# Optimization experiments

Hardware: AMD Instinct MI355X
Metric: run time of the kernel (lower is better)

The kernel has to match this reference:

```python
import jax, jax.numpy as jnp
import numpy as np

T, B, E, H = 1024, 2, 1024, 16
D = E // H  # head_dim = 64
R = 2 * T - 1  # relative position range


def setup_inputs() -> dict:
    key = jax.random.key(0)
    ks = jax.random.split(key, 8)
    std = (2.0 / (E + E)) ** 0.5  # matches nn.init.normal_ std in reset_parameters
    return {
        "x": jax.random.normal(ks[0], (T, B, E), jnp.float32),
        "pos": jax.random.normal(ks[1], (R, 1, E), jnp.float32),
        "in_proj_weight": jax.random.normal(ks[2], (3 * E, E), jnp.float32) * std,
        "in_proj_bias": jnp.zeros((3 * E,), jnp.float32),
        "pos_proj_weight": jax.random.normal(ks[3], (E, E), jnp.float32) * std,
        "pos_proj_bias": jnp.zeros((E,), jnp.float32),
        "out_proj_weight": jax.random.normal(ks[4], (E, E), jnp.float32) * std,
        "out_proj_bias": jnp.zeros((E,), jnp.float32),
        "r_w_bias": jax.random.normal(ks[5], (H, D), jnp.float32) * 0.02,
        "r_r_bias": jax.random.normal(ks[6], (H, D), jnp.float32) * 0.02,
    }


def _rel_shift(x):
    """Transformer-XL relative shift. x: [b, h, q, r] -> shifted [b, h, q, r]."""
    b, h, q, r = x.shape
    zp = jnp.zeros((b, h, q, 1), x.dtype)
    xp = jnp.concatenate([zp, x], axis=3)          # [b, h, q, r+1]
    xp = xp.reshape(b, h, r + 1, q)[:, :, 1:, :]   # drop first row
    return xp.reshape(b, h, q, r)


def reference(x, pos, in_proj_weight, in_proj_bias, pos_proj_weight,
              pos_proj_bias, out_proj_weight, out_proj_bias, r_w_bias, r_r_bias):
    t, b, e = x.shape
    h, d = r_w_bias.shape
    # fused QKV projection: [T, B, 3E]
    qkv = x @ in_proj_weight.T + in_proj_bias
    q, k, v = jnp.split(qkv, 3, axis=-1)
    q = q.reshape(t, b, h, d)
    k = k.reshape(t, b, h, d)
    v = v.reshape(t, b, h, d)
    # position projection: [R, 1, E] -> [R, h, d]
    p = (pos @ pos_proj_weight.T + pos_proj_bias).reshape(-1, h, d)
    scale = 1.0 / jnp.sqrt(jnp.asarray(d, x.dtype))
    # content score AC: (q + r_w_bias) @ k^T
    ac = jnp.einsum('tbhd,sbhd->bhts', q + r_w_bias, k)
    # position score BD: (q + r_r_bias) @ pos^T, then relative shift
    bd = jnp.einsum('tbhd,rhd->bhtr', q + r_r_bias, p)
    bd = _rel_shift(bd)[..., :t]                    # keep klen columns
    attn = jax.nn.softmax((ac + bd) * scale, axis=-1)  # [b, h, t, s]
    ctx = jnp.einsum('bhts,sbhd->tbhd', attn, v).reshape(t, b, e)
    return ctx @ out_proj_weight.T + out_proj_bias
```

## Files before the change

### kernel.cpp

```cpp
#include <hip/hip_runtime.h>
#include <hip/hip_bf16.h>

#define TT 1024
#define BB 2
#define EE 1024
#define HH 16
#define DD 64
#define RR 2047
#define TB (TT * BB)
#define E3 (3 * EE)

#define AS1 __attribute__((address_space(1)))
#define AS3 __attribute__((address_space(3)))

typedef __attribute__((ext_vector_type(4))) float f32x4;
typedef __attribute__((ext_vector_type(8))) short s16x8;

static __device__ __forceinline__ short f2bf(float x) {
  unsigned u = __builtin_bit_cast(unsigned, x);
  unsigned r = (u + 0x7FFFu + ((u >> 16) & 1u)) >> 16;
  return (short)r;
}
static __device__ __forceinline__ float bf2f(short x) {
  unsigned u = ((unsigned)(unsigned short)x) << 16;
  return __builtin_bit_cast(float, u);
}
static __device__ __forceinline__ float bperm(int idx, float v) {
  return __builtin_bit_cast(float,
      __builtin_amdgcn_ds_bpermute(idx, __builtin_bit_cast(int, v)));
}
static __device__ __forceinline__ float exp2g(float x) {
  return __builtin_amdgcn_exp2f(x);
}

__global__ __launch_bounds__(256) void cvt_all(
    const float* __restrict__ x, const float* __restrict__ in_w,
    const float* __restrict__ pos, const float* __restrict__ pos_w,
    const float* __restrict__ out_w,
    short* __restrict__ xb, short* __restrict__ inwb, short* __restrict__ posb,
    short* __restrict__ poswb, short* __restrict__ outwb) {
  const long M1 = 1 << 20;
  long off = (long)(blockIdx.x * 256 + threadIdx.x) * 8;
  const float* src; short* dst; long nsrc;
  if (off < 2 * M1)      { src = x;     dst = xb;    nsrc = 2 * M1; }
  else if (off < 5 * M1) { off -= 2 * M1; src = in_w;  dst = inwb;  nsrc = 3 * M1; }
  else if (off < 7 * M1) { off -= 5 * M1; src = pos;   dst = posb;  nsrc = (long)RR * EE; }
  else if (off < 8 * M1) { off -= 7 * M1; src = pos_w; dst = poswb; nsrc = M1; }
  else                   { off -= 8 * M1; src = out_w; dst = outwb; nsrc = M1; }
  s16x8 o;
  if (off + 8 <= nsrc) {
    f32x4 a = *(const f32x4*)&src[off];
    f32x4 c = *(const f32x4*)&src[off + 4];
    #pragma unroll
    for (int j = 0; j < 4; ++j) { o[j] = f2bf(a[j]); o[4 + j] = f2bf(c[j]); }
  } else {
    #pragma unroll
    for (int j = 0; j < 8; ++j) o[j] = 0;
  }
  *(s16x8*)&dst[off] = o;
}

#define GBK 64

template <int BM, int BN, int WR, int WC, int OUT_BF16>
__device__ __forceinline__ void gemm_body(
    const short* __restrict__ A, const short* __restrict__ W,
    const float* __restrict__ bias, void* __restrict__ Cout,
    int M, int N, int K, int m0, int n0,
    short* __restrict__ vtout, int vtflag) {
  __shared__ __align__(16) short lA[2][BM * GBK];
  __shared__ __align__(16) short lB[2][BN * GBK];
  constexpr int MT = BM / WR / 16;
  constexpr int NT = BN / WC / 16;

  const int tid = threadIdx.x;
  const int lane = tid & 63;
  const int wv = tid >> 6;
  const int g = lane >> 4, cc = lane & 15;
  const int wr = wv / WC, wc = wv % WC;

  f32x4 acc[MT][NT];
  #pragma unroll
  for (int i = 0; i < MT; ++i)
    #pragma unroll
    for (int j = 0; j < NT; ++j) acc[i][j] = (f32x4){0.f, 0.f, 0.f, 0.f};

  auto stage = [&](int kk, int buf) {
    #pragma unroll
    for (int s = 0; s < BM / 32; ++s) {
      int c = s * 256 + tid;
      int row = c >> 3, c8 = c & 7;
      int k8 = c8 ^ (row & 7);
      __builtin_amdgcn_global_load_lds(
          (const AS1 void*)(A + (size_t)(m0 + row) * K + kk + k8 * 8),
          (AS3 void*)&lA[buf][c * 8], 16, 0, 0);
    }
    #pragma unroll
    for (int s = 0; s < BN / 32; ++s) {
      int c = s * 256 + tid;
      int row = c >> 3, c8 = c & 7;
      int k8 = c8 ^ (row & 7);
      __builtin_amdgcn_global_load_lds(
          (const AS1 void*)(W + (size_t)(n0 + row) * K + kk + k8 * 8),
          (AS3 void*)&lB[buf][c * 8], 16, 0, 0);
    }
  };

  int cur = 0;
  const int nt = K / GBK;
  stage(0, 0);

  #pragma unroll 1
  for (int t = 0; t < nt; ++t) {
    __syncthreads();
    if (t + 1 < nt) stage((t + 1) * GBK, cur ^ 1);

    s16x8 af[MT][2], bf[NT][2];
    #pragma unroll
    for (int mt = 0; mt < MT; ++mt) {
      int row = (BM / WR) * wr + 16 * mt + cc;
      #pragma unroll
      for (int kh = 0; kh < 2; ++kh)
        af[mt][kh] = *(const s16x8*)&lA[cur][row * GBK + (((4 * kh + g) ^ (row & 7)) * 8)];
    }
    #pragma unroll
    for (int ntc = 0; ntc < NT; ++ntc) {
      int col = (BN / WC) * wc + 16 * ntc + cc;
      #pragma unroll
      for (int kh = 0; kh < 2; ++kh)
        bf[ntc][kh] = *(const s16x8*)&lB[cur][col * GBK + (((4 * kh + g) ^ (col & 7)) * 8)];
    }
    #pragma unroll
    for (int kh = 0; kh < 2; ++kh)
      #pragma unroll
      for (int mt = 0; mt < MT; ++mt)
        #pragma unroll
        for (int ntc = 0; ntc < NT; ++ntc)
          acc[mt][ntc] = __builtin_amdgcn_mfma_f32_16x16x32_bf16(
              af[mt][kh], bf[ntc][kh], acc[mt][ntc], 0, 0, 0);
    cur ^= 1;
  }

  #pragma unroll
  for (int ntc = 0; ntc < NT; ++ntc) {
    int col = n0 + (BN / WC) * wc + 16 * ntc + cc;
    float bv = bias[col];
    #pragma unroll
    for (int mt = 0; mt < MT; ++mt)
      #pragma unroll
      for (int r = 0; r < 4; ++r) {
        int rowg = m0 + (BM / WR) * wr + 16 * mt + 4 * g + r;
        float val = acc[mt][ntc][r] + bv;
        if (OUT_BF16) {
          if (vtflag) {
            const int cv = col - 2048;
            const int hh = cv >> 6, dd = cv & 63;
            vtout[((size_t)((rowg & 1) * 16 + hh) * 64 + dd) * TT + (rowg >> 1)] =
                f2bf(val);
          } else {
            ((short*)Cout)[(size_t)rowg * N + col] = f2bf(val);
          }
        } else {
          ((float*)Cout)[(size_t)rowg * N + col] = val;
        }
      }
  }
}

__global__ __launch_bounds__(256) void gemm_qkv_pos(
    const short* __restrict__ xb, const short* __restrict__ inwb,
    const float* __restrict__ in_b, short* __restrict__ qkvb,
    const short* __restrict__ posb, const short* __restrict__ poswb,
    const float* __restrict__ pos_b, short* __restrict__ pb,
    short* __restrict__ vTb) {
  const int bid = blockIdx.x;
  const short *A, *W; const float* bias; short* C; int N, m0, n0, vtf;
  if (bid < 384) {
    A = xb; W = inwb; bias = in_b; C = qkvb; N = E3;
    n0 = (bid % 24) * 128; m0 = (bid / 24) * 128;
    vtf = (n0 >= 2048) ? 1 : 0;
  } else {
    const int i = bid - 384;
    A = posb; W = poswb; bias = pos_b; C = pb; N = EE;
    n0 = (i % 8) * 128; m0 = (i / 8) * 128;
    vtf = 0;
  }
  gemm_body<128, 128, 2, 2, 1>(A, W, bias, C, TB, N, EE, m0, n0, vTb, vtf);
}

__global__ __launch_bounds__(256) void gemm_out(
    const short* __restrict__ ctxb, const short* __restrict__ outwb,
    const float* __restrict__ out_b, float* __restrict__ out) {
  gemm_body<128, 64, 4, 1, 0>(ctxb, outwb, out_b, out, TB, EE, EE,
                              blockIdx.y * 128, blockIdx.x * 64, nullptr, 0);
}

__global__ __launch_bounds__(512, 4) void rel_attn_mfma9(
    const short* __restrict__ qkvb,
    const short* __restrict__ pb,
    const short* __restrict__ vT,
    const float* __restrict__ rwb,
    const float* __restrict__ rrb,
    short* __restrict__ ctxb) {
  __shared__ __align__(16) char arena[68608];

  const int tid = threadIdx.x;
  const int wv = tid >> 6;
  const int qsub = wv & 3, ksub = wv >> 2;
  const int lane = tid & 63;
  const int g = lane >> 4, cc = lane & 15;

  const int bid = blockIdx.x;
  const int bh = (bid & 7) * 4 + (bid >> 7);
  const int qx = (bid >> 3) & 15;
  const int iq0 = qx * 64;
  const int b = bh >> 4, h = bh & 15;
  const int hoff = h * DD;
  const int n0p = 15 - qx;

  short* sPm = (short*)(arena + 57344 + wv * 1280);

  const float qscale = 0.125f * 1.44269504088896f;
  s16x8 qw[2], qr[2];
  #pragma unroll
  for (int kh = 0; kh < 2; ++kh) {
    const int d0 = 32 * kh + 8 * g;
    const short* qp = qkvb + (size_t)((iq0 + 16 * qsub + cc) * BB + b) * E3 + hoff + d0;
    const float* rw = rwb + hoff + d0;
    const float* rr = rrb + hoff + d0;
    s16x8 qv = *(const s16x8*)qp;
    #pragma unroll
    for (int j = 0; j < 8; ++j) {
      float q = bf2f(qv[j]);
      qw[kh][j] = f2bf((q + rw[j]) * qscale);
      qr[kh][j] = f2bf((q + rr[j]) * qscale);
    }
  }

  f32x4 O[4];
  #pragma unroll
  for (int dt = 0; dt < 4; ++dt) O[dt] = (f32x4){0.f, 0.f, 0.f, 0.f};
  float mrun[4], lpart[4];
  #pragma unroll
  for (int r = 0; r < 4; ++r) { mrun[r] = -1e30f; lpart[r] = 0.f; }

#define STAGE_KV(t_, buf_)                                                     \
  {                                                                            \
    const int j0s = (t_) * 64;                                                 \
    const int row = tid >> 3, c8 = tid & 7;                                    \
    const int swz = (c8 ^ (row & 7)) * 8;                                      \
    __builtin_amdgcn_global_load_lds(                                          \
        (const AS1 void*)(qkvb + (size_t)((j0s + row) * BB + b) * E3 + EE + hoff + swz), \
        (AS3 void*)(arena + (buf_) * 8192 + tid * 16), 16, 0, 0);              \
    __builtin_amdgcn_global_load_lds(                                          \
        (const AS1 void*)(vT + (size_t)(bh * DD + row) * TT + j0s + swz),      \
        (AS3 void*)(arena + 16384 + (buf_) * 8192 + tid * 16), 16, 0, 0);      \
  }
#define STAGE_P(p_)                                                            \
  {                                                                            \
    const int row = tid >> 3, c8 = tid & 7;                                    \
    const int swz = (c8 ^ (row & 7)) * 8;                                      \
    __builtin_amdgcn_global_load_lds(                                          \
        (const AS1 void*)(pb + (size_t)((p_) * 64 + row) * EE + hoff + swz),   \
        (AS3 void*)(arena + 32768 + ((p_) % 3) * 8192 + tid * 16), 16, 0, 0);  \
  }

  int cur = 0;
  int sl0 = n0p % 3, sl1 = (n0p + 1) % 3;
  STAGE_KV(0, 0);
  STAGE_P(n0p);
  STAGE_P(n0p + 1);

  #pragma unroll 1
  for (int t = 0; t < 16; ++t) {
    __syncthreads();
    if (t + 1 < 16) {
      STAGE_KV(t + 1, cur ^ 1);
      STAGE_P(n0p + t + 2);
    }

    short* ldsK = (short*)(arena + cur * 8192);
    short* ldsV = (short*)(arena + 16384 + cur * 8192);

    s16x8 kf[2][2];
    #pragma unroll
    for (int ct = 0; ct < 2; ++ct)
      #pragma unroll
      for (int kh = 0; kh < 2; ++kh) {
        const int row = 32 * ksub + 16 * ct + cc;
        kf[ct][kh] = *(const s16x8*)&ldsK[row * 64 + (((g + 4 * kh) ^ (row & 7)) * 8)];
      }

    f32x4 S[2];
    #pragma unroll
    for (int ct = 0; ct < 2; ++ct) {
      S[ct] = (f32x4){0.f, 0.f, 0.f, 0.f};
      #pragma unroll
      for (int kh = 0; kh < 2; ++kh)
        S[ct] = __builtin_amdgcn_mfma_f32_16x16x32_bf16(qw[kh], kf[ct][kh], S[ct], 0, 0, 0);
    }

    const int bbase = 32 * ksub - 16 * qsub + 48;
    f32x4 bt[3];
    #pragma unroll
    for (int ut = 0; ut < 3; ++ut) {
      const int rel = bbase + 16 * ut + cc;
      const int rr = rel & 63;
      const short* pp_ = (const short*)(arena + 32768 +
                                        ((rel >= 64) ? sl1 : sl0) * 8192);
      bt[ut] = (f32x4){0.f, 0.f, 0.f, 0.f};
      #pragma unroll
      for (int kh = 0; kh < 2; ++kh) {
        s16x8 pf = *(const s16x8*)&pp_[rr * 64 + (((g + 4 * kh) ^ (rr & 7)) * 8)];
        bt[ut] = __builtin_amdgcn_mfma_f32_16x16x32_bf16(qr[kh], pf, bt[ut], 0, 0, 0);
      }
    }
    #pragma unroll
    for (int r = 0; r < 4; ++r) {
      const int usub = cc + 15 - 4 * g - r;
      const int idx = ((lane & 48) | (usub & 15)) << 2;
      const float va = bperm(idx, bt[0][r]);
      const float vb = bperm(idx, bt[1][r]);
      const float vc = bperm(idx, bt[2][r]);
      const bool hi = usub >= 16;
      S[0][r] += hi ? vb : va;
      S[1][r] += hi ? vc : vb;
    }

    float mx[4];
    #pragma unroll
    for (int r = 0; r < 4; ++r) mx[r] = fmaxf(S[0][r], S[1][r]);
    const bool need = (mx[0] > mrun[0]) || (mx[1] > mrun[1]) ||
                      (mx[2] > mrun[2]) || (mx[3] > mrun[3]);
    if (__any(need)) {
      #pragma unroll
      for (int msk = 1; msk < 16; msk <<= 1)
        #pragma unroll
        for (int r = 0; r < 4; ++r) mx[r] = fmaxf(mx[r], __shfl_xor(mx[r], msk, 64));
      #pragma unroll
      for (int r = 0; r < 4; ++r) {
        const float mn = fmaxf(mrun[r], mx[r]);
        const float f = exp2g(mrun[r] - mn);
        mrun[r] = mn;
        lpart[r] *= f;
        #pragma unroll
        for (int dt = 0; dt < 4; ++dt) O[dt][r] *= f;
      }
    }
    #pragma unroll
    for (int r = 0; r < 4; ++r) {
      S[0][r] = exp2g(S[0][r] - mrun[r]);
      S[1][r] = exp2g(S[1][r] - mrun[r]);
      lpart[r] += S[0][r] + S[1][r];
    }

    #pragma unroll
    for (int ct = 0; ct < 2; ++ct)
      #pragma unroll
      for (int r = 0; r < 4; ++r)
        sPm[(4 * g + r) * 40 + 16 * ct + cc] = f2bf(S[ct][r]);

    s16x8 pa = *(const s16x8*)&sPm[cc * 40 + 8 * g];

    #pragma unroll
    for (int dt = 0; dt < 4; ++dt) {
      const int row = 16 * dt + cc;
      s16x8 vf = *(const s16x8*)&ldsV[row * 64 + (((4 * ksub + g) ^ (row & 7)) * 8)];
      O[dt] = __builtin_amdgcn_mfma_f32_16x16x32_bf16(pa, vf, O[dt], 0, 0, 0);
    }

    cur ^= 1;
    const int sln = (sl1 + 1) - (((sl1 + 1) >= 3) ? 3 : 0);
    sl0 = sl1;
    sl1 = sln;
  }
#undef STAGE_KV
#undef STAGE_P

  #pragma unroll
  for (int msk = 1; msk < 16; msk <<= 1)
    #pragma unroll
    for (int r = 0; r < 4; ++r) lpart[r] += __shfl_xor(lpart[r], msk, 64);

  __syncthreads();

  float* sOw = (float*)(arena + wv * 4352);
  #pragma unroll
  for (int dt = 0; dt < 4; ++dt)
    #pragma unroll
    for (int r = 0; r < 4; ++r)
      sOw[(4 * g + r) * 68 + 16 * dt + cc] = O[dt][r];
  float* sML = (float*)(arena + 67584);
  if (cc == 0) {
    #pragma unroll
    for (int r = 0; r < 4; ++r) {
      sML[wv * 32 + (4 * g + r)] = mrun[r];
      sML[wv * 32 + 16 + (4 * g + r)] = lpart[r];
    }
  }
  __syncthreads();

  const int ii = tid >> 3;
  const int ii_l = ii & 15;
  const int w0 = ii >> 4, w1 = w0 + 4;
  const int c0 = (tid & 7) * 8;
  const float m0 = sML[w0 * 32 + ii_l], l0 = sML[w0 * 32 + 16 + ii_l];
  const float m1 = sML[w1 * 32 + ii_l], l1 = sML[w1 * 32 + 16 + ii_l];
  const float M = fmaxf(m0, m1);
  const float f0 = exp2g(m0 - M), f1 = exp2g(m1 - M);
  const float rinv = 1.0f / (f0 * l0 + f1 * l1);
  const float* sO0 = (const float*)(arena + w0 * 4352);
  const float* sO1 = (const float*)(arena + w1 * 4352);
  s16x8 ov;
  #pragma unroll
  for (int jj = 0; jj < 8; ++jj) {
    const float val = (f0 * sO0[ii_l * 68 + c0 + jj] + f1 * sO1[ii_l * 68 + c0 + jj]) * rinv;
    ov[jj] = f2bf(val);
  }
  *(s16x8*)(ctxb + (size_t)((iq0 + ii) * BB + b) * EE + hoff + c0) = ov;
}

extern "C" void kernel_launch(void* const* d_in, const int* in_sizes, int n_in,
                              void* d_out, int out_size, void* d_ws, size_t ws_size,
                              hipStream_t stream) {
  const float* x      = (const float*)d_in[0];
  const float* pos    = (const float*)d_in[1];
  const float* in_w   = (const float*)d_in[2];
  const float* in_b   = (const float*)d_in[3];
  const float* pos_w  = (const float*)d_in[4];
  const float* pos_b  = (const float*)d_in[5];
  const float* out_w  = (const float*)d_in[6];
  const float* out_b  = (const float*)d_in[7];
  const float* r_w    = (const float*)d_in[8];
  const float* r_r    = (const float*)d_in[9];
  float* out = (float*)d_out;

  const size_t M1 = 1024 * 1024;
  short* xb    = (short*)d_ws;
  short* inwb  = xb    + 2 * M1;
  short* posb  = inwb  + 3 * M1;
  short* poswb = posb  + 2 * M1;
  short* outwb = poswb + 1 * M1;
  short* qkvb  = outwb + 1 * M1;
  short* pb    = qkvb  + 6 * M1;
  short* ctxb  = pb    + 2 * M1;
  short* vTb   = ctxb  + 2 * M1;

  cvt_all<<<dim3(4608), dim3(256), 0, stream>>>(
      x, in_w, pos, pos_w, out_w, xb, inwb, posb, poswb, outwb);

  gemm_qkv_pos<<<dim3(512), dim3(256), 0, stream>>>(
      xb, inwb, in_b, qkvb, posb, poswb, pos_b, pb, vTb);

  rel_attn_mfma9<<<dim3(512), dim3(512), 0, stream>>>(
      qkvb, pb, vTb, r_w, r_r, ctxb);

  gemm_out<<<dim3(EE / 64, TB / 128), dim3(256), 0, stream>>>(
      ctxb, outwb, out_b, out);
}
```

Measured before the change: 102.6 us.

## Give each attention wave two query tiles with 256-thread blocks

The relative attention kernel drops from 8 waves to 4 per block. Each wave now handles 32 query rows as two 16-row tiles instead of one, so K, V and position fragments read from LDS are reused across both tiles, and the position fragments are shared between overlapping BD tiles (4 loads instead of 6). Staging loops are doubled so fewer threads cover the same tiles. The cost is higher register pressure and fewer waves per block to hide latency.

```diff
diff --git a/kernel.cpp b/kernel.cpp
--- a/kernel.cpp
+++ b/kernel.cpp
@@ -195,7 +195,7 @@
                               blockIdx.y * 128, blockIdx.x * 64, nullptr, 0);
 }
 
-__global__ __launch_bounds__(512, 4) void rel_attn_mfma9(
+__global__ __launch_bounds__(256) void rel_attn_mfma10(
     const short* __restrict__ qkvb,
     const short* __restrict__ pb,
     const short* __restrict__ vT,
@@ -206,7 +206,7 @@
 
   const int tid = threadIdx.x;
   const int wv = tid >> 6;
-  const int qsub = wv & 3, ksub = wv >> 2;
+  const int qsub = wv >> 1, ksub = wv & 1;
   const int lane = tid & 63;
   const int g = lane >> 4, cc = lane & 15;
 
@@ -218,51 +218,65 @@
   const int hoff = h * DD;
   const int n0p = 15 - qx;
 
-  short* sPm = (short*)(arena + 57344 + wv * 1280);
+  short* sPm = (short*)(arena + 57344 + wv * 2560);
 
   const float qscale = 0.125f * 1.44269504088896f;
-  s16x8 qw[2], qr[2];
-  #pragma unroll
-  for (int kh = 0; kh < 2; ++kh) {
-    const int d0 = 32 * kh + 8 * g;
-    const short* qp = qkvb + (size_t)((iq0 + 16 * qsub + cc) * BB + b) * E3 + hoff + d0;
-    const float* rw = rwb + hoff + d0;
-    const float* rr = rrb + hoff + d0;
-    s16x8 qv = *(const s16x8*)qp;
-    #pragma unroll
-    for (int j = 0; j < 8; ++j) {
-      float q = bf2f(qv[j]);
-      qw[kh][j] = f2bf((q + rw[j]) * qscale);
-      qr[kh][j] = f2bf((q + rr[j]) * qscale);
-    }
-  }
-
-  f32x4 O[4];
-  #pragma unroll
-  for (int dt = 0; dt < 4; ++dt) O[dt] = (f32x4){0.f, 0.f, 0.f, 0.f};
-  float mrun[4], lpart[4];
-  #pragma unroll
-  for (int r = 0; r < 4; ++r) { mrun[r] = -1e30f; lpart[r] = 0.f; }
+  s16x8 qw[2][2], qr[2][2];
+  #pragma unroll
+  for (int qt = 0; qt < 2; ++qt)
+    #pragma unroll
+    for (int kh = 0; kh < 2; ++kh) {
+      const int d0 = 32 * kh + 8 * g;
+      const short* qp = qkvb + (size_t)((iq0 + 32 * qsub + 16 * qt + cc) * BB + b) * E3 + hoff + d0;
+      const float* rw = rwb + hoff + d0;
+      const float* rr = rrb + hoff + d0;
+      s16x8 qv = *(const s16x8*)qp;
+      #pragma unroll
+      for (int j = 0; j < 8; ++j) {
+        float q = bf2f(qv[j]);
+        qw[qt][kh][j] = f2bf((q + rw[j]) * qscale);
+        qr[qt][kh][j] = f2bf((q + rr[j]) * qscale);
+      }
+    }
+
+  f32x4 O[2][4];
+  #pragma unroll
+  for (int qt = 0; qt < 2; ++qt)
+    #pragma unroll
+    for (int dt = 0; dt < 4; ++dt) O[qt][dt] = (f32x4){0.f, 0.f, 0.f, 0.f};
+  float mrun[2][4], lpart[2][4];
+  #pragma unroll
+  for (int qt = 0; qt < 2; ++qt)
+    #pragma unroll
+    for (int r = 0; r < 4; ++r) { mrun[qt][r] = -1e30f; lpart[qt][r] = 0.f; }
 
 #define STAGE_KV(t_, buf_)                                                     \
   {                                                                            \
     const int j0s = (t_) * 64;                                                 \
-    const int row = tid >> 3, c8 = tid & 7;                                    \
-    const int swz = (c8 ^ (row & 7)) * 8;                                      \
-    __builtin_amdgcn_global_load_lds(                                          \
-        (const AS1 void*)(qkvb + (size_t)((j0s + row) * BB + b) * E3 + EE + hoff + swz), \
-        (AS3 void*)(arena + (buf_) * 8192 + tid * 16), 16, 0, 0);              \
-    __builtin_amdgcn_global_load_lds(                                          \
-        (const AS1 void*)(vT + (size_t)(bh * DD + row) * TT + j0s + swz),      \
-        (AS3 void*)(arena + 16384 + (buf_) * 8192 + tid * 16), 16, 0, 0);      \
+    _Pragma("unroll")                                                          \
+    for (int s2 = 0; s2 < 2; ++s2) {                                           \
+      const int c = tid + 256 * s2;                                            \
+      const int row = c >> 3, c8 = c & 7;                                      \
+      const int swz = (c8 ^ (row & 7)) * 8;                                    \
+      __builtin_amdgcn_global_load_lds(                                        \
+          (const AS1 void*)(qkvb + (size_t)((j0s + row) * BB + b) * E3 + EE + hoff + swz), \
+          (AS3 void*)(arena + (buf_) * 8192 + c * 16), 16, 0, 0);              \
+      __builtin_amdgcn_global_load_lds(                                        \
+          (const AS1 void*)(vT + (size_t)(bh * DD + row) * TT + j0s + swz),    \
+          (AS3 void*)(arena + 16384 + (buf_) * 8192 + c * 16), 16, 0, 0);      \
+    }                                                                          \
   }
 #define STAGE_P(p_)                                                            \
   {                                                                            \
-    const int row = tid >> 3, c8 = tid & 7;                                    \
-    const int swz = (c8 ^ (row & 7)) * 8;                                      \
-    __builtin_amdgcn_global_load_lds(                                          \
-        (const AS1 void*)(pb + (size_t)((p_) * 64 + row) * EE + hoff + swz),   \
-        (AS3 void*)(arena + 32768 + ((p_) % 3) * 8192 + tid * 16), 16, 0, 0);  \
+    _Pragma("unroll")                                                          \
+    for (int s2 = 0; s2 < 2; ++s2) {                                           \
+      const int c = tid + 256 * s2;                                            \
+      const int row = c >> 3, c8 = c & 7;                                      \
+      const int swz = (c8 ^ (row & 7)) * 8;                                    \
+      __builtin_amdgcn_global_load_lds(                                        \
+          (const AS1 void*)(pb + (size_t)((p_) * 64 + row) * EE + hoff + swz), \
+          (AS3 void*)(arena + 32768 + ((p_) % 3) * 8192 + c * 16), 16, 0, 0);  \
+    }                                                                          \
   }
 
   int cur = 0;
@@ -290,83 +304,116 @@
         const int row = 32 * ksub + 16 * ct + cc;
         kf[ct][kh] = *(const s16x8*)&ldsK[row * 64 + (((g + 4 * kh) ^ (row & 7)) * 8)];
       }
-
-    f32x4 S[2];
-    #pragma unroll
-    for (int ct = 0; ct < 2; ++ct) {
-      S[ct] = (f32x4){0.f, 0.f, 0.f, 0.f};
-      #pragma unroll
-      for (int kh = 0; kh < 2; ++kh)
-        S[ct] = __builtin_amdgcn_mfma_f32_16x16x32_bf16(qw[kh], kf[ct][kh], S[ct], 0, 0, 0);
-    }
-
-    const int bbase = 32 * ksub - 16 * qsub + 48;
-    f32x4 bt[3];
-    #pragma unroll
-    for (int ut = 0; ut < 3; ++ut) {
-      const int rel = bbase + 16 * ut + cc;
+    s16x8 vf[4];
+    #pragma unroll
+    for (int dt = 0; dt < 4; ++dt) {
+      const int row = 16 * dt + cc;
+      vf[dt] = *(const s16x8*)&ldsV[row * 64 + (((4 * ksub + g) ^ (row & 7)) * 8)];
+    }
+
+    f32x4 S[2][2];
+    #pragma unroll
+    for (int qt = 0; qt < 2; ++qt)
+      #pragma unroll
+      for (int ct = 0; ct < 2; ++ct) {
+        S[qt][ct] = (f32x4){0.f, 0.f, 0.f, 0.f};
+        #pragma unroll
+        for (int kh = 0; kh < 2; ++kh)
+          S[qt][ct] = __builtin_amdgcn_mfma_f32_16x16x32_bf16(
+              qw[qt][kh], kf[ct][kh], S[qt][ct], 0, 0, 0);
+      }
+
+    const int bbase_u = 32 * (ksub - qsub) + 32;
+    s16x8 pf[4][2];
+    #pragma unroll
+    for (int ut = 0; ut < 4; ++ut) {
+      const int rel = bbase_u + 16 * ut + cc;
       const int rr = rel & 63;
       const short* pp_ = (const short*)(arena + 32768 +
                                         ((rel >= 64) ? sl1 : sl0) * 8192);
-      bt[ut] = (f32x4){0.f, 0.f, 0.f, 0.f};
-      #pragma unroll
-      for (int kh = 0; kh < 2; ++kh) {
-        s16x8 pf = *(const s16x8*)&pp_[rr * 64 + (((g + 4 * kh) ^ (rr & 7)) * 8)];
-        bt[ut] = __builtin_amdgcn_mfma_f32_16x16x32_bf16(qr[kh], pf, bt[ut], 0, 0, 0);
-      }
-    }
+      #pragma unroll
+      for (int kh = 0; kh < 2; ++kh)
+        pf[ut][kh] = *(const s16x8*)&pp_[rr * 64 + (((g + 4 * kh) ^ (rr & 7)) * 8)];
+    }
+    f32x4 bt[2][3];
+    #pragma unroll
+    for (int qt = 0; qt < 2; ++qt)
+      #pragma unroll
+      for (int m = 0; m < 3; ++m) {
+        const int ut = m + 1 - qt;
+        bt[qt][m] = (f32x4){0.f, 0.f, 0.f, 0.f};
+        #pragma unroll
+        for (int kh = 0; kh < 2; ++kh)
+          bt[qt][m] = __builtin_amdgcn_mfma_f32_16x16x32_bf16(
+              qr[qt][kh], pf[ut][kh], bt[qt][m], 0, 0, 0);
+      }
     #pragma unroll
     for (int r = 0; r < 4; ++r) {
-      const int usub = cc + 15 - 4 * g - r;
-      const int idx = ((lane & 48) | (usub & 15)) << 2;
-      const float va = bperm(idx, bt[0][r]);
-      const float vb = bperm(idx, bt[1][r]);
-      const float vc = bperm(idx, bt[2][r]);
-      const bool hi = usub >= 16;
-      S[0][r] += hi ? vb : va;
-      S[1][r] += hi ? vc : vb;
-    }
-
-    float mx[4];
-    #pragma unroll
-    for (int r = 0; r < 4; ++r) mx[r] = fmaxf(S[0][r], S[1][r]);
-    const bool need = (mx[0] > mrun[0]) || (mx[1] > mrun[1]) ||
-                      (mx[2] > mrun[2]) || (mx[3] > mrun[3]);
-    if (__any(need)) {
+      const int u0 = cc + 15 - 4 * g - r;
+      const int idx = ((lane & 48) | (u0 & 15)) << 2;
+      const bool hi = u0 >= 16;
+      #pragma unroll
+      for (int qt = 0; qt < 2; ++qt) {
+        const float va = bperm(idx, bt[qt][0][r]);
+        const float vb = bperm(idx, bt[qt][1][r]);
+        const float vc = bperm(idx, bt[qt][2][r]);
+        S[qt][0][r] += hi ? vb : va;
+        S[qt][1][r] += hi ? vc : vb;
+      }
+    }
+
+    float mx[2][4];
+    bool needv = false;
+    #pragma unroll
+    for (int qt = 0; qt < 2; ++qt)
+      #pragma unroll
+      for (int r = 0; r < 4; ++r) {
+        mx[qt][r] = fmaxf(S[qt][0][r], S[qt][1][r]);
+        needv = needv || (mx[qt][r] > mrun[qt][r]);
+      }
+    if (__any(needv)) {
       #pragma unroll
       for (int msk = 1; msk < 16; msk <<= 1)
         #pragma unroll
-        for (int r = 0; r < 4; ++r) mx[r] = fmaxf(mx[r], __shfl_xor(mx[r], msk, 64));
+        for (int qt = 0; qt < 2; ++qt)
+          #pragma unroll
+          for (int r = 0; r < 4; ++r)
+            mx[qt][r] = fmaxf(mx[qt][r], __shfl_xor(mx[qt][r], msk, 64));
+      #pragma unroll
+      for (int qt = 0; qt < 2; ++qt)
+        #pragma unroll
+        for (int r = 0; r < 4; ++r) {
+          const float mn = fmaxf(mrun[qt][r], mx[qt][r]);
+          const float f = exp2g(mrun[qt][r] - mn);
+          mrun[qt][r] = mn;
+          lpart[qt][r] *= f;
+          #pragma unroll
+          for (int dt = 0; dt < 4; ++dt) O[qt][dt][r] *= f;
+        }
+    }
+    #pragma unroll
+    for (int qt = 0; qt < 2; ++qt)
       #pragma unroll
       for (int r = 0; r < 4; ++r) {
-        const float mn = fmaxf(mrun[r], mx[r]);
-        const float f = exp2g(mrun[r] - mn);
-        mrun[r] = mn;
-        lpart[r] *= f;
+        S[qt][0][r] = exp2g(S[qt][0][r] - mrun[qt][r]);
+        S[qt][1][r] = exp2g(S[qt][1][r] - mrun[qt][r]);
+        lpart[qt][r] += S[qt][0][r] + S[qt][1][r];
+      }
+
+    #pragma unroll
+    for (int qt = 0; qt < 2; ++qt)
+      #pragma unroll
+      for (int ct = 0; ct < 2; ++ct)
         #pragma unroll
-        for (int dt = 0; dt < 4; ++dt) O[dt][r] *= f;
-      }
-    }
-    #pragma unroll
-    for (int r = 0; r < 4; ++r) {
-      S[0][r] = exp2g(S[0][r] - mrun[r]);
-      S[1][r] = exp2g(S[1][r] - mrun[r]);
-      lpart[r] += S[0][r] + S[1][r];
-    }
-
-    #pragma unroll
-    for (int ct = 0; ct < 2; ++ct)
-      #pragma unroll
-      for (int r = 0; r < 4; ++r)
-        sPm[(4 * g + r) * 40 + 16 * ct + cc] = f2bf(S[ct][r]);
-
-    s16x8 pa = *(const s16x8*)&sPm[cc * 40 + 8 * g];
-
-    #pragma unroll
-    for (int dt = 0; dt < 4; ++dt) {
-      const int row = 16 * dt + cc;
-      s16x8 vf = *(const s16x8*)&ldsV[row * 64 + (((4 * ksub + g) ^ (row & 7)) * 8)];
-      O[dt] = __builtin_amdgcn_mfma_f32_16x16x32_bf16(pa, vf, O[dt], 0, 0, 0);
+        for (int r = 0; r < 4; ++r)
+          sPm[(16 * qt + 4 * g + r) * 40 + 16 * ct + cc] = f2bf(S[qt][ct][r]);
+
+    #pragma unroll
+    for (int qt = 0; qt < 2; ++qt) {
+      s16x8 pa = *(const s16x8*)&sPm[(16 * qt + cc) * 40 + 8 * g];
+      #pragma unroll
+      for (int dt = 0; dt < 4; ++dt)
+        O[qt][dt] = __builtin_amdgcn_mfma_f32_16x16x32_bf16(pa, vf[dt], O[qt][dt], 0, 0, 0);
     }
 
     cur ^= 1;
@@ -380,44 +427,57 @@
   #pragma unroll
   for (int msk = 1; msk < 16; msk <<= 1)
     #pragma unroll
-    for (int r = 0; r < 4; ++r) lpart[r] += __shfl_xor(lpart[r], msk, 64);
+    for (int qt = 0; qt < 2; ++qt)
+      #pragma unroll
+      for (int r = 0; r < 4; ++r)
+        lpart[qt][r] += __shfl_xor(lpart[qt][r], msk, 64);
 
   __syncthreads();
 
-  float* sOw = (float*)(arena + wv * 4352);
-  #pragma unroll
-  for (int dt = 0; dt < 4; ++dt)
-    #pragma unroll
-    for (int r = 0; r < 4; ++r)
-      sOw[(4 * g + r) * 68 + 16 * dt + cc] = O[dt][r];
+  float* sOw = (float*)(arena + wv * 8704);
+  #pragma unroll
+  for (int qt = 0; qt < 2; ++qt)
+    #pragma unroll
+    for (int dt = 0; dt < 4; ++dt)
+      #pragma unroll
+      for (int r = 0; r < 4; ++r)
+        sOw[(16 * qt + 4 * g + r) * 68 + 16 * dt + cc] = O[qt][dt][r];
   float* sML = (float*)(arena + 67584);
   if (cc == 0) {
     #pragma unroll
-    for (int r = 0; r < 4; ++r) {
-      sML[wv * 32 + (4 * g + r)] = mrun[r];
-      sML[wv * 32 + 16 + (4 * g + r)] = lpart[r];
-    }
+    for (int qt = 0; qt < 2; ++qt)
+      #pragma unroll
+      for (int r = 0; r < 4; ++r) {
+        sML[wv * 64 + (16 * qt + 4 * g + r)] = mrun[qt][r];
+        sML[wv * 64 + 32 + (16 * qt + 4 * g + r)] = lpart[qt][r];
+      }
   }
   __syncthreads();
 
-  const int ii = tid >> 3;
-  const int ii_l = ii & 15;
-  const int w0 = ii >> 4, w1 = w0 + 4;
-  const int c0 = (tid & 7) * 8;
-  const float m0 = sML[w0 * 32 + ii_l], l0 = sML[w0 * 32 + 16 + ii_l];
-  const float m1 = sML[w1 * 32 + ii_l], l1 = sML[w1 * 32 + 16 + ii_l];
+  const int ii = tid >> 2;
+  const int rloc = ii & 31;
+  const int qs = ii >> 5;
+  const int w0 = 2 * qs, w1 = w0 + 1;
+  const int c0 = (tid & 3) * 16;
+  const float m0 = sML[w0 * 64 + rloc], l0 = sML[w0 * 64 + 32 + rloc];
+  const float m1 = sML[w1 * 64 + rloc], l1 = sML[w1 * 64 + 32 + rloc];
   const float M = fmaxf(m0, m1);
   const float f0 = exp2g(m0 - M), f1 = exp2g(m1 - M);
   const float rinv = 1.0f / (f0 * l0 + f1 * l1);
-  const float* sO0 = (const float*)(arena + w0 * 4352);
-  const float* sO1 = (const float*)(arena + w1 * 4352);
-  s16x8 ov;
-  #pragma unroll
-  for (int jj = 0; jj < 8; ++jj) {
-    const float val = (f0 * sO0[ii_l * 68 + c0 + jj] + f1 * sO1[ii_l * 68 + c0 + jj]) * rinv;
-    ov[jj] = f2bf(val);
-  }
-  *(s16x8*)(ctxb + (size_t)((iq0 + ii) * BB + b) * EE + hoff + c0) = ov;
+  const float* sO0 = (const float*)(arena + w0 * 8704);
+  const float* sO1 = (const float*)(arena + w1 * 8704);
+  short* dst = ctxb + (size_t)((iq0 + ii) * BB + b) * EE + hoff + c0;
+  #pragma unroll
+  for (int half = 0; half < 2; ++half) {
+    s16x8 ov;
+    #pragma unroll
+    for (int jj = 0; jj < 8; ++jj) {
+      const int col = c0 + half * 8 + jj;
+      const float val = (f0 * sO0[rloc * 68 + col] + f1 * sO1[rloc * 68 + col]) * rinv;
+      ov[jj] = f2bf(val);
+    }
+    *(s16x8*)(dst + half * 8) = ov;
+  }
 }
 
 extern "C" void kernel_launch(void* const* d_in, const int* in_sizes, int n_in,
@@ -452,7 +512,7 @@
   gemm_qkv_pos<<<dim3(512), dim3(256), 0, stream>>>(
       xb, inwb, in_b, qkvb, posb, poswb, pos_b, pb, vTb);
 
-  rel_attn_mfma9<<<dim3(512), dim3(512), 0, stream>>>(
+  rel_attn_mfma10<<<dim3(512), dim3(256), 0, stream>>>(
       qkvb, pb, vTb, r_w, r_r, ctxb);
 
   gemm_out<<<dim3(EE / 64, TB / 128), dim3(256), 0, stream>>>(
```

Measured after the change: 108.6 us. 5.8% more time.
